# Performance work log

Measured on AMD Instinct MI355X. Metric: run time of the kernel, lower is better.

## Reference

```python
import jax, jax.numpy as jnp
import numpy as np

NUM_HEADS = 8
GROUPS = 32  # min(32, 512 // 4)
EPS = 1e-5


def group_norm(y, gamma, beta):
    B, C, L = y.shape
    yg = y.reshape(B, GROUPS, -1)  # [B, G, (C//G)*L]
    mu = yg.mean(-1, keepdims=True)
    var = yg.var(-1, keepdims=True)
    yn = ((yg - mu) * jax.lax.rsqrt(var + EPS)).reshape(B, C, L)
    return yn * gamma[:, None] + beta[:, None]


def setup_inputs() -> dict:
    key = jax.random.key(0)
    ks = jax.random.split(key, 5)
    B, C, L = 4, 512, 2048
    return {
        "x": jax.random.normal(ks[0], (B, C, L), dtype=jnp.float32),
        "Wqkv": jax.random.normal(ks[1], (3 * C, C), dtype=jnp.float32) * (C ** -0.5),
        "bqkv": jax.random.normal(ks[2], (3 * C,), dtype=jnp.float32) * 0.01,
        "Wproj": jax.random.normal(ks[3], (C, C), dtype=jnp.float32) * (C ** -0.5),
        "bproj": jax.random.normal(ks[4], (C,), dtype=jnp.float32) * 0.01,
        "gamma": jnp.ones((C,), dtype=jnp.float32),
        "beta": jnp.zeros((C,), dtype=jnp.float32),
    }


def reference(x, Wqkv, bqkv, Wproj, bproj, gamma, beta):
    B, C, L = x.shape
    H = NUM_HEADS
    D = C // H
    # 1x1 Conv1d == channel-mixing matmul
    qkv = jnp.einsum('oc,bcl->bol', Wqkv, x) + bqkv[:, None]  # [B, 3C, L]
    qkv = qkv.reshape(B, 3, H, D, L)
    q, k, v = qkv[:, 0], qkv[:, 1], qkv[:, 2]
    q = jnp.clip(q, -10.0, 10.0)
    k = jnp.clip(k, -10.0, 10.0)
    v = jnp.clip(v, -10.0, 10.0)
    scale = D ** -0.5
    attn = jnp.einsum('bhdi,bhdj->bhij', q, k) * scale  # [B, H, L, L]
    attn = jnp.clip(attn, -10.0, 10.0)
    attn = jax.nn.softmax(attn, axis=-1)
    # NaN fallback: replace whole attn with identity if any NaN (matches torch branch)
    has_nan = jnp.isnan(attn).any()
    attn = jnp.where(has_nan, jnp.eye(L, dtype=x.dtype), attn)
    out = jnp.einsum('bhij,bhdj->bhdi', attn, v)  # [B, H, D, L]
    out = out.reshape(B, C, L)
    out = jnp.einsum('oc,bcl->bol', Wproj, out) + bproj[:, None]
    return group_norm(out + x, gamma, beta)
```

## Files before the change

kernel.cpp:

```cpp
#include <hip/hip_runtime.h>
#include <cstddef>

#define B_ 4
#define C_ 512
#define L_ 2048

typedef __attribute__((ext_vector_type(8))) short  short8;
typedef __attribute__((ext_vector_type(4))) float  f32x4;
typedef __attribute__((ext_vector_type(4))) unsigned short us4;

#define AS1 __attribute__((address_space(1)))
#define AS3 __attribute__((address_space(3)))

__device__ __forceinline__ float clip10(float v){ return fminf(fmaxf(v,-10.0f),10.0f); }

__device__ __forceinline__ unsigned short f2bf(float f){
  union { float f; unsigned u; } v; v.f = f;
  unsigned r = v.u + 0x7fffu + ((v.u >> 16) & 1u);
  return (unsigned short)(r >> 16);
}
__device__ __forceinline__ unsigned pk_tr(float lo, float hi){
  return __builtin_amdgcn_perm(__float_as_uint(hi), __float_as_uint(lo), 0x07060302u);
}
__device__ __forceinline__ float bf2f(unsigned short u){
  return __uint_as_float(((unsigned)u)<<16);
}
__device__ __forceinline__ void gl16(const void* g, void* l){
  __builtin_amdgcn_global_load_lds((const AS1 unsigned*)g, (AS3 unsigned*)l, 16, 0, 0);
}

__global__ __launch_bounds__(256) void prep_k(
    const float* __restrict__ x, const float* __restrict__ Wq,
    const float* __restrict__ Wp, unsigned short* __restrict__ xT,
    unsigned short* __restrict__ Wqb, unsigned short* __restrict__ Wpb,
    float* __restrict__ part)
{
  const int blk = blockIdx.x;
  const int t = threadIdx.x;
  if (blk < 4096){
    __shared__ float tile[32][33];
    const int b = blk>>10, rem = blk&1023;
    const int c0 = (rem>>6)*32, l0 = (rem&63)*32;
    const int cr = t>>3, lc = (t&7)*4;
    const float4 v = *(const float4*)(x + ((size_t)b*C_ + c0+cr)*L_ + l0 + lc);
    tile[cr][lc]=v.x; tile[cr][lc+1]=v.y; tile[cr][lc+2]=v.z; tile[cr][lc+3]=v.w;
    __syncthreads();
    const int lr = t>>3, cc = (t&7)*4;
    const us4 o = { f2bf(tile[cc][lr]), f2bf(tile[cc+1][lr]),
                    f2bf(tile[cc+2][lr]), f2bf(tile[cc+3][lr]) };
    *(us4*)(xT + ((size_t)b*L_ + l0+lr)*C_ + c0 + cc) = o;
  } else if (blk < 5120){
    const int i = (blk-4096)*256 + t;
    const int NQ = 1536*512/4;
    const float* src; unsigned short* dst; int j;
    if (i < NQ){ src = Wq; dst = Wqb; j = i; }
    else       { src = Wp; dst = Wpb; j = i - NQ; }
    const float4 v = *(const float4*)(src + (size_t)j*4);
    const us4 o = { f2bf(v.x), f2bf(v.y), f2bf(v.z), f2bf(v.w) };
    *(us4*)(dst + (size_t)j*4) = o;
  } else {
    part[t] = 0.f;
  }
}

template<int MODE>
__global__ __launch_bounds__(256) void mfma_gemm(
    const unsigned short* __restrict__ Wb, const unsigned short* __restrict__ Bin,
    const float* __restrict__ bias, const float* __restrict__ xres,
    unsigned short* __restrict__ qT, unsigned short* __restrict__ kT,
    unsigned short* __restrict__ vN, float* __restrict__ yout,
    float* __restrict__ part)
{
  __shared__ unsigned short SA[128*64];
  __shared__ unsigned short SB[128*64];
  const int t = threadIdx.x;
  const int b = blockIdx.z;
  const int mb = blockIdx.y, n0 = blockIdx.x*128, m0 = mb*128;
  const int lane = t&63, w = t>>6, wm = w>>1, wn = w&1;
  const int n = lane&15, q4 = lane>>4;

  f32x4 acc[4][4];
#pragma unroll
  for (int i=0;i<4;i++)
#pragma unroll
    for (int j=0;j<4;j++) acc[i][j] = (f32x4){0.f,0.f,0.f,0.f};

  const unsigned short* Arow = Wb + (size_t)m0*512;
  const unsigned short* Brow = Bin + ((size_t)b*L_ + n0)*512;

  for (int kt=0; kt<8; kt++){
    const int k0 = kt*64;
    __syncthreads();
#pragma unroll
    for (int i=0;i<4;i++){
      const int ch = t + 256*i;
      const int row = ch>>3, lc = (ch&7) ^ (row&7);
      gl16(Arow + (size_t)row*512 + k0 + lc*8, &SA[ch*8]);
      gl16(Brow + (size_t)row*512 + k0 + lc*8, &SB[ch*8]);
    }
    __syncthreads();
#pragma unroll
    for (int kk=0;kk<2;kk++){
      short8 aF[4], bF[4];
      const int pc = ((kk*4+q4) ^ (n&7))*8;
#pragma unroll
      for (int mt=0;mt<4;mt++) aF[mt] = *(const short8*)&SA[(wm*64+mt*16+n)*64 + pc];
#pragma unroll
      for (int nt=0;nt<4;nt++) bF[nt] = *(const short8*)&SB[(wn*64+nt*16+n)*64 + pc];
#pragma unroll
      for (int mt=0;mt<4;mt++)
#pragma unroll
        for (int nt=0;nt<4;nt++)
          acc[mt][nt] = __builtin_amdgcn_mfma_f32_16x16x32_bf16(aF[mt], bF[nt], acc[mt][nt], 0,0,0);
    }
  }

  const float QS = 0.180336880f;
#pragma unroll
  for (int mt=0;mt<4;mt++){
    const int obase = m0 + wm*64 + mt*16 + q4*4;
    const float b0=bias[obase], b1=bias[obase+1], b2=bias[obase+2], b3=bias[obase+3];
    float gs=0.f, gq=0.f;
#pragma unroll
    for (int nt=0;nt<4;nt++){
      const int l = n0 + wn*64 + nt*16 + n;
      float r0=acc[mt][nt][0]+b0, r1=acc[mt][nt][1]+b1,
            r2=acc[mt][nt][2]+b2, r3=acc[mt][nt][3]+b3;
      if (MODE==0){
        r0=clip10(r0); r1=clip10(r1); r2=clip10(r2); r3=clip10(r3);
        const int typ = mb>>2;
        const int oin = obase - typ*512;
        if (typ < 2){
          if (typ==0){ r0*=QS; r1*=QS; r2*=QS; r3*=QS; }
          unsigned short* dst = (typ==0) ? qT : kT;
          const us4 o = { f2bf(r0), f2bf(r1), f2bf(r2), f2bf(r3) };
          *(us4*)&dst[((size_t)b*L_ + l)*512 + oin] = o;
        } else {
          unsigned short* dst = vN + ((size_t)b*512 + oin)*L_ + l;
          dst[0]=f2bf(r0); dst[(size_t)L_]=f2bf(r1);
          dst[(size_t)2*L_]=f2bf(r2); dst[(size_t)3*L_]=f2bf(r3);
        }
      } else {
        const float* xp = xres + ((size_t)b*512 + obase)*L_ + l;
        const float y0=r0+xp[0], y1=r1+xp[(size_t)L_],
                    y2=r2+xp[(size_t)2*L_], y3=r3+xp[(size_t)3*L_];
        float* dst = yout + ((size_t)b*512 + obase)*L_ + l;
        dst[0]=y0; dst[(size_t)L_]=y1; dst[(size_t)2*L_]=y2; dst[(size_t)3*L_]=y3;
        gs += (y0+y1)+(y2+y3);
        gq += (y0*y0+y1*y1)+(y2*y2+y3*y3);
      }
    }
    if (MODE==1){
#pragma unroll
      for (int off=1; off<64; off<<=1){
        gs += __shfl_xor(gs, off);
        gq += __shfl_xor(gq, off);
      }
      if (lane==0){
        const int g = mb*8 + wm*4 + mt;
        atomicAdd(&part[(b*32+g)*2+0], gs);
        atomicAdd(&part[(b*32+g)*2+1], gq);
      }
    }
  }
}

#define PP 72

__global__ __launch_bounds__(256,4) void attn_v9(
    const unsigned short* __restrict__ qT, const unsigned short* __restrict__ kT,
    const unsigned short* __restrict__ vN,
    unsigned short* __restrict__ Opart, float* __restrict__ den)
{
  __shared__ unsigned short s_k[64*64];
  __shared__ unsigned short s_v[64*64];
  __shared__ unsigned short s_p[128*PP];
  const int t  = threadIdx.x;
  const int io = blockIdx.x>>1, half = blockIdx.x&1;
  const int i0 = io*128;
  const int h  = blockIdx.y, b = blockIdx.z;
  const int lane = t&63, w = t>>6, n = lane&15, q4 = lane>>4;
  const int idx = ((b*8+h)*16+io)*2 + half;

  const unsigned short* kb0 = kT + (size_t)b*L_*512 + h*64;
  const unsigned short* vb  = vN + ((size_t)b*512 + h*64)*L_;

  short8 qf[2][2];
#pragma unroll
  for (int mt=0; mt<2; mt++)
#pragma unroll
    for (int kk=0; kk<2; kk++)
      qf[mt][kk] = *(const short8*)(qT + ((size_t)b*L_ + i0 + w*32 + mt*16 + n)*512
                                       + h*64 + kk*32 + q4*8);

  short8 ones;
#pragma unroll
  for (int i=0;i<8;i++) ones[i] = (short)0x3F80;

  f32x4 oacc[2][4];
  f32x4 oden[2];
#pragma unroll
  for (int mt=0;mt<2;mt++){ oden[mt]=(f32x4){0.f,0.f,0.f,0.f};
#pragma unroll
    for (int dt=0;dt<4;dt++) oacc[mt][dt]=(f32x4){0.f,0.f,0.f,0.f}; }

  const float LIM = 14.4269504089f;
  const int jbeg = half*1024, jend = jbeg+1024;

  for (int j0=jbeg; j0<jend; j0+=64){
    __syncthreads();
#pragma unroll
    for (int i=0;i<2;i++){
      const int ch = t + 256*i, row = ch>>3, lc = (ch&7)^(row&7);
      gl16(kb0 + (size_t)(j0+row)*512 + lc*8, &s_k[ch*8]);
      gl16(vb  + (size_t)row*L_ + j0 + lc*8,  &s_v[ch*8]);
    }
    __syncthreads();

    f32x4 sacc[2][4];
#pragma unroll
    for (int mt=0;mt<2;mt++)
#pragma unroll
      for (int jt=0;jt<4;jt++) sacc[mt][jt]=(f32x4){0.f,0.f,0.f,0.f};
#pragma unroll
    for (int kk=0;kk<2;kk++){
      const int pc = ((kk*4+q4) ^ (n&7))*8;
      short8 aK[4];
#pragma unroll
      for (int jt=0;jt<4;jt++) aK[jt] = *(const short8*)&s_k[(jt*16+n)*64 + pc];
#pragma unroll
      for (int mt=0;mt<2;mt++)
#pragma unroll
        for (int jt=0;jt<4;jt++)
          sacc[mt][jt] = __builtin_amdgcn_mfma_f32_16x16x32_bf16(aK[jt], qf[mt][kk], sacc[mt][jt], 0,0,0);
    }

#pragma unroll
    for (int mt=0;mt<2;mt++)
#pragma unroll
      for (int jt=0;jt<4;jt++){
        const float e0 = __builtin_amdgcn_exp2f(__builtin_amdgcn_fmed3f(sacc[mt][jt][0],-LIM,LIM));
        const float e1 = __builtin_amdgcn_exp2f(__builtin_amdgcn_fmed3f(sacc[mt][jt][1],-LIM,LIM));
        const float e2 = __builtin_amdgcn_exp2f(__builtin_amdgcn_fmed3f(sacc[mt][jt][2],-LIM,LIM));
        const float e3 = __builtin_amdgcn_exp2f(__builtin_amdgcn_fmed3f(sacc[mt][jt][3],-LIM,LIM));
        const unsigned long long pv =
            (unsigned long long)pk_tr(e0,e1) | ((unsigned long long)pk_tr(e2,e3)<<32);
        *(unsigned long long*)&s_p[(w*32 + mt*16 + n)*PP + jt*16 + q4*4] = pv;
      }

#pragma unroll
    for (int kk=0;kk<2;kk++){
      const int pcv = ((kk*4+q4) ^ (n&7))*8;
      short8 bV[4], pA[2];
#pragma unroll
      for (int dt=0;dt<4;dt++) bV[dt] = *(const short8*)&s_v[(dt*16+n)*64 + pcv];
#pragma unroll
      for (int mt=0;mt<2;mt++)
        pA[mt] = *(const short8*)&s_p[(w*32 + mt*16 + n)*PP + kk*32 + q4*8];
#pragma unroll
      for (int mt=0;mt<2;mt++){
#pragma unroll
        for (int dt=0;dt<4;dt++)
          oacc[mt][dt] = __builtin_amdgcn_mfma_f32_16x16x32_bf16(pA[mt], bV[dt], oacc[mt][dt], 0,0,0);
        oden[mt] = __builtin_amdgcn_mfma_f32_16x16x32_bf16(pA[mt], ones, oden[mt], 0,0,0);
      }
    }
  }

  if (n == 0){
#pragma unroll
    for (int mt=0;mt<2;mt++)
#pragma unroll
      for (int r=0;r<4;r++)
        den[(size_t)idx*128 + w*32 + mt*16 + q4*4 + r] = oden[mt][r];
  }

#pragma unroll
  for (int mt=0;mt<2;mt++)
#pragma unroll
    for (int dt=0;dt<4;dt++)
#pragma unroll
      for (int r=0;r<4;r++)
        Opart[(size_t)idx*8192 + (w*32 + mt*16 + q4*4 + r)*64 + dt*16 + n]
            = f2bf(oacc[mt][dt][r]);
}

__global__ __launch_bounds__(256) void attn_combine(
    const unsigned short* __restrict__ Opart, const float* __restrict__ den,
    unsigned short* __restrict__ attnT)
{
  __shared__ float s_inv[128];
  const int io = blockIdx.x, h = blockIdx.y, b = blockIdx.z;
  const int t = threadIdx.x;
  const int base = ((b*8+h)*16+io)*2;
  if (t < 128)
    s_inv[t] = 1.0f/(den[(size_t)base*128 + t] + den[(size_t)(base+1)*128 + t]);
  __syncthreads();
  const unsigned short* O0 = Opart + (size_t)base*8192;
  const unsigned short* O1 = O0 + 8192;
#pragma unroll
  for (int it=0; it<8; it++){
    const int chunk = it*256 + t;
    const int i = chunk>>4, c4 = (chunk&15)*4;
    const us4 a = *(const us4*)&O0[i*64 + c4];
    const us4 c = *(const us4*)&O1[i*64 + c4];
    const float inv = s_inv[i];
    const us4 o = { f2bf((bf2f(a[0])+bf2f(c[0]))*inv),
                    f2bf((bf2f(a[1])+bf2f(c[1]))*inv),
                    f2bf((bf2f(a[2])+bf2f(c[2]))*inv),
                    f2bf((bf2f(a[3])+bf2f(c[3]))*inv) };
    *(us4*)&attnT[((size_t)b*L_ + io*128 + i)*512 + h*64 + c4] = o;
  }
}

__global__ __launch_bounds__(256) void gn_apply(
    const float* __restrict__ y, const float* __restrict__ part,
    const float* __restrict__ gamma, const float* __restrict__ beta,
    float* __restrict__ out)
{
  const int blk = blockIdx.x;
  const int b = blk>>7, g = (blk>>2)&31, s = blk&3;
  const float sum = part[(b*32+g)*2+0];
  const float sq  = part[(b*32+g)*2+1];
  const float mu = sum*(1.0f/32768.0f);
  const float rs = rsqrtf(sq*(1.0f/32768.0f) - mu*mu + 1e-5f);
  const size_t base = ((size_t)b*C_ + g*16)*L_ + s*512;
  const int t = threadIdx.x;
#pragma unroll
  for (int i=0;i<8;i++){
    const int e = i*256 + t;
    const int row = e>>7;
    const size_t off = base + (size_t)row*L_ + (e&127)*4;
    const int c = g*16 + row;
    const float ga = gamma[c], be = beta[c];
    const float4 vy=*(const float4*)(y+off);
    float4 r;
    r.x=(vy.x-mu)*rs*ga+be;
    r.y=(vy.y-mu)*rs*ga+be;
    r.z=(vy.z-mu)*rs*ga+be;
    r.w=(vy.w-mu)*rs*ga+be;
    *(float4*)(out+off)=r;
  }
}

extern "C" void kernel_launch(void* const* d_in, const int* in_sizes, int n_in,
                              void* d_out, int out_size, void* d_ws, size_t ws_size,
                              hipStream_t stream)
{
  (void)in_sizes; (void)n_in; (void)out_size; (void)ws_size;
  const float* x     = (const float*)d_in[0];
  const float* Wqkv  = (const float*)d_in[1];
  const float* bqkv  = (const float*)d_in[2];
  const float* Wproj = (const float*)d_in[3];
  const float* bproj = (const float*)d_in[4];
  const float* gamma = (const float*)d_in[5];
  const float* beta  = (const float*)d_in[6];
  float* out = (float*)d_out;
  char* ws = (char*)d_ws;

  const size_t MB = 1024*1024;
  unsigned short* qT    = (unsigned short*)(ws);
  unsigned short* kT    = (unsigned short*)(ws +  8*MB);
  unsigned short* vN    = (unsigned short*)(ws + 16*MB);
  unsigned short* attnT = (unsigned short*)(ws + 24*MB);
  unsigned short* xT    = (unsigned short*)(ws + 32*MB);
  float*          den   = (float*)        (ws + 41*MB);
  unsigned short* Wqb   = (unsigned short*)(ws + 42*MB);
  unsigned short* Wpb   = (unsigned short*)(ws + 44*MB);
  float*          y     = (float*)        (ws + 45*MB);
  unsigned short* Opart = (unsigned short*)(ws + 45*MB);
  float*          part  = (float*)        (ws + 61*MB);

  prep_k      <<<dim3(5121),   256,0,stream>>>(x, Wqkv, Wproj, xT, Wqb, Wpb, part);
  mfma_gemm<0><<<dim3(16,12,4),256,0,stream>>>(Wqb, xT,    bqkv , nullptr, qT,kT,vN, nullptr, nullptr);
  attn_v9     <<<dim3(32,8,4), 256,0,stream>>>(qT, kT, vN, Opart, den);
  attn_combine<<<dim3(16,8,4), 256,0,stream>>>(Opart, den, attnT);
  mfma_gemm<1><<<dim3(16, 4,4),256,0,stream>>>(Wpb, attnT, bproj, x, nullptr,nullptr,nullptr, y, part);
  gn_apply    <<<dim3(512),    256,0,stream>>>(y, part, gamma, beta, out);
}
```

Baseline: 189.0 us.

## Split attention waves over key halves and vectorize V stores in QKV GEMM

The attention kernel now gives each wave 64 query rows and half of each 64-key tile, rather than 32 query rows and the full tile. This halves the K fragment loads per wave and reuses each Q fragment across more MFMAs. A shared-memory reduction at the end merges the two key-half partial outputs and denominators, and the occupancy hint drops from 4 to 3 blocks to fit the larger register footprint. The QKV GEMM also swaps MFMA operands for the V blocks, so the transposed V output is written as contiguous 4-element vector stores instead of strided scalar ones.

```diff
diff --git a/kernel.cpp b/kernel.cpp
--- a/kernel.cpp
+++ b/kernel.cpp
@@ -78,6 +78,7 @@
   const int mb = blockIdx.y, n0 = blockIdx.x*128, m0 = mb*128;
   const int lane = t&63, w = t>>6, wm = w>>1, wn = w&1;
   const int n = lane&15, q4 = lane>>4;
+  const bool VSWAP = (MODE==0) && (mb>=8);
 
   f32x4 acc[4][4];
 #pragma unroll
@@ -107,15 +108,39 @@
       for (int mt=0;mt<4;mt++) aF[mt] = *(const short8*)&SA[(wm*64+mt*16+n)*64 + pc];
 #pragma unroll
       for (int nt=0;nt<4;nt++) bF[nt] = *(const short8*)&SB[(wn*64+nt*16+n)*64 + pc];
-#pragma unroll
-      for (int mt=0;mt<4;mt++)
-#pragma unroll
-        for (int nt=0;nt<4;nt++)
-          acc[mt][nt] = __builtin_amdgcn_mfma_f32_16x16x32_bf16(aF[mt], bF[nt], acc[mt][nt], 0,0,0);
+      if (VSWAP){
+#pragma unroll
+        for (int mt=0;mt<4;mt++)
+#pragma unroll
+          for (int nt=0;nt<4;nt++)
+            acc[mt][nt] = __builtin_amdgcn_mfma_f32_16x16x32_bf16(bF[nt], aF[mt], acc[mt][nt], 0,0,0);
+      } else {
+#pragma unroll
+        for (int mt=0;mt<4;mt++)
+#pragma unroll
+          for (int nt=0;nt<4;nt++)
+            acc[mt][nt] = __builtin_amdgcn_mfma_f32_16x16x32_bf16(aF[mt], bF[nt], acc[mt][nt], 0,0,0);
+      }
     }
   }
 
   const float QS = 0.180336880f;
+  if (VSWAP){
+#pragma unroll
+    for (int mt=0;mt<4;mt++){
+      const int o = m0 + wm*64 + mt*16 + n;
+      const float bv = bias[o];
+#pragma unroll
+      for (int nt=0;nt<4;nt++){
+        const int l = n0 + wn*64 + nt*16 + q4*4;
+        const float r0=clip10(acc[mt][nt][0]+bv), r1=clip10(acc[mt][nt][1]+bv),
+                    r2=clip10(acc[mt][nt][2]+bv), r3=clip10(acc[mt][nt][3]+bv);
+        const us4 ov = { f2bf(r0), f2bf(r1), f2bf(r2), f2bf(r3) };
+        *(us4*)&vN[((size_t)b*512 + (o-1024))*L_ + l] = ov;
+      }
+    }
+    return;
+  }
 #pragma unroll
   for (int mt=0;mt<4;mt++){
     const int obase = m0 + wm*64 + mt*16 + q4*4;
@@ -130,16 +155,10 @@
         r0=clip10(r0); r1=clip10(r1); r2=clip10(r2); r3=clip10(r3);
         const int typ = mb>>2;
         const int oin = obase - typ*512;
-        if (typ < 2){
-          if (typ==0){ r0*=QS; r1*=QS; r2*=QS; r3*=QS; }
-          unsigned short* dst = (typ==0) ? qT : kT;
-          const us4 o = { f2bf(r0), f2bf(r1), f2bf(r2), f2bf(r3) };
-          *(us4*)&dst[((size_t)b*L_ + l)*512 + oin] = o;
-        } else {
-          unsigned short* dst = vN + ((size_t)b*512 + oin)*L_ + l;
-          dst[0]=f2bf(r0); dst[(size_t)L_]=f2bf(r1);
-          dst[(size_t)2*L_]=f2bf(r2); dst[(size_t)3*L_]=f2bf(r3);
-        }
+        if (typ==0){ r0*=QS; r1*=QS; r2*=QS; r3*=QS; }
+        unsigned short* dst = (typ==0) ? qT : kT;
+        const us4 o = { f2bf(r0), f2bf(r1), f2bf(r2), f2bf(r3) };
+        *(us4*)&dst[((size_t)b*L_ + l)*512 + oin] = o;
       } else {
         const float* xp = xres + ((size_t)b*512 + obase)*L_ + l;
         const float y0=r0+xp[0], y1=r1+xp[(size_t)L_],
@@ -166,46 +185,50 @@
 }
 
 #define PP 72
-
-__global__ __launch_bounds__(256,4) void attn_v9(
+#define EXP 66
+
+__global__ __launch_bounds__(256,3) void attn_v12(
     const unsigned short* __restrict__ qT, const unsigned short* __restrict__ kT,
     const unsigned short* __restrict__ vN,
     unsigned short* __restrict__ Opart, float* __restrict__ den)
 {
-  __shared__ unsigned short s_k[64*64];
-  __shared__ unsigned short s_v[64*64];
-  __shared__ unsigned short s_p[128*PP];
+  __shared__ unsigned short smem[2*64*64 + 128*PP];
+  unsigned short* s_k = smem;
+  unsigned short* s_v = smem + 4096;
+  unsigned short* s_p = smem + 8192;
   const int t  = threadIdx.x;
   const int io = blockIdx.x>>1, half = blockIdx.x&1;
   const int i0 = io*128;
   const int h  = blockIdx.y, b = blockIdx.z;
   const int lane = t&63, w = t>>6, n = lane&15, q4 = lane>>4;
+  const int wi = w&1, wj = w>>1;
   const int idx = ((b*8+h)*16+io)*2 + half;
 
   const unsigned short* kb0 = kT + (size_t)b*L_*512 + h*64;
   const unsigned short* vb  = vN + ((size_t)b*512 + h*64)*L_;
 
-  short8 qf[2][2];
-#pragma unroll
-  for (int mt=0; mt<2; mt++)
+  short8 qf[4][2];
+#pragma unroll
+  for (int mt=0; mt<4; mt++)
 #pragma unroll
     for (int kk=0; kk<2; kk++)
-      qf[mt][kk] = *(const short8*)(qT + ((size_t)b*L_ + i0 + w*32 + mt*16 + n)*512
+      qf[mt][kk] = *(const short8*)(qT + ((size_t)b*L_ + i0 + wi*64 + mt*16 + n)*512
                                        + h*64 + kk*32 + q4*8);
 
   short8 ones;
 #pragma unroll
   for (int i=0;i<8;i++) ones[i] = (short)0x3F80;
 
-  f32x4 oacc[2][4];
-  f32x4 oden[2];
-#pragma unroll
-  for (int mt=0;mt<2;mt++){ oden[mt]=(f32x4){0.f,0.f,0.f,0.f};
+  f32x4 oacc[4][4];
+  f32x4 oden[4];
+#pragma unroll
+  for (int mt=0;mt<4;mt++){ oden[mt]=(f32x4){0.f,0.f,0.f,0.f};
 #pragma unroll
     for (int dt=0;dt<4;dt++) oacc[mt][dt]=(f32x4){0.f,0.f,0.f,0.f}; }
 
   const float LIM = 14.4269504089f;
   const int jbeg = half*1024, jend = jbeg+1024;
+  const int prow = (wi*64 + n)*PP + wj*32;
 
   for (int j0=jbeg; j0<jend; j0+=64){
     __syncthreads();
@@ -217,48 +240,48 @@
     }
     __syncthreads();
 
-    f32x4 sacc[2][4];
-#pragma unroll
-    for (int mt=0;mt<2;mt++)
-#pragma unroll
-      for (int jt=0;jt<4;jt++) sacc[mt][jt]=(f32x4){0.f,0.f,0.f,0.f};
+    f32x4 sacc[4][2];
+#pragma unroll
+    for (int mt=0;mt<4;mt++)
+#pragma unroll
+      for (int jt2=0;jt2<2;jt2++) sacc[mt][jt2]=(f32x4){0.f,0.f,0.f,0.f};
 #pragma unroll
     for (int kk=0;kk<2;kk++){
       const int pc = ((kk*4+q4) ^ (n&7))*8;
-      short8 aK[4];
-#pragma unroll
-      for (int jt=0;jt<4;jt++) aK[jt] = *(const short8*)&s_k[(jt*16+n)*64 + pc];
-#pragma unroll
-      for (int mt=0;mt<2;mt++)
-#pragma unroll
-        for (int jt=0;jt<4;jt++)
-          sacc[mt][jt] = __builtin_amdgcn_mfma_f32_16x16x32_bf16(aK[jt], qf[mt][kk], sacc[mt][jt], 0,0,0);
-    }
-
-#pragma unroll
-    for (int mt=0;mt<2;mt++)
-#pragma unroll
-      for (int jt=0;jt<4;jt++){
-        const float e0 = __builtin_amdgcn_exp2f(__builtin_amdgcn_fmed3f(sacc[mt][jt][0],-LIM,LIM));
-        const float e1 = __builtin_amdgcn_exp2f(__builtin_amdgcn_fmed3f(sacc[mt][jt][1],-LIM,LIM));
-        const float e2 = __builtin_amdgcn_exp2f(__builtin_amdgcn_fmed3f(sacc[mt][jt][2],-LIM,LIM));
-        const float e3 = __builtin_amdgcn_exp2f(__builtin_amdgcn_fmed3f(sacc[mt][jt][3],-LIM,LIM));
+      short8 aK[2];
+#pragma unroll
+      for (int jt2=0;jt2<2;jt2++)
+        aK[jt2] = *(const short8*)&s_k[(wj*32+jt2*16+n)*64 + pc];
+#pragma unroll
+      for (int mt=0;mt<4;mt++)
+#pragma unroll
+        for (int jt2=0;jt2<2;jt2++)
+          sacc[mt][jt2] = __builtin_amdgcn_mfma_f32_16x16x32_bf16(aK[jt2], qf[mt][kk], sacc[mt][jt2], 0,0,0);
+    }
+
+#pragma unroll
+    for (int mt=0;mt<4;mt++)
+#pragma unroll
+      for (int jt2=0;jt2<2;jt2++){
+        const float e0 = __builtin_amdgcn_exp2f(__builtin_amdgcn_fmed3f(sacc[mt][jt2][0],-LIM,LIM));
+        const float e1 = __builtin_amdgcn_exp2f(__builtin_amdgcn_fmed3f(sacc[mt][jt2][1],-LIM,LIM));
+        const float e2 = __builtin_amdgcn_exp2f(__builtin_amdgcn_fmed3f(sacc[mt][jt2][2],-LIM,LIM));
+        const float e3 = __builtin_amdgcn_exp2f(__builtin_amdgcn_fmed3f(sacc[mt][jt2][3],-LIM,LIM));
         const unsigned long long pv =
             (unsigned long long)pk_tr(e0,e1) | ((unsigned long long)pk_tr(e2,e3)<<32);
-        *(unsigned long long*)&s_p[(w*32 + mt*16 + n)*PP + jt*16 + q4*4] = pv;
-      }
-
-#pragma unroll
-    for (int kk=0;kk<2;kk++){
-      const int pcv = ((kk*4+q4) ^ (n&7))*8;
-      short8 bV[4], pA[2];
+        *(unsigned long long*)&s_p[prow + mt*16*PP + jt2*16 + q4*4] = pv;
+      }
+
+    {
+      const int pcv = ((wj*4+q4) ^ (n&7))*8;
+      short8 bV[4], pA[4];
 #pragma unroll
       for (int dt=0;dt<4;dt++) bV[dt] = *(const short8*)&s_v[(dt*16+n)*64 + pcv];
 #pragma unroll
-      for (int mt=0;mt<2;mt++)
-        pA[mt] = *(const short8*)&s_p[(w*32 + mt*16 + n)*PP + kk*32 + q4*8];
-#pragma unroll
-      for (int mt=0;mt<2;mt++){
+      for (int mt=0;mt<4;mt++)
+        pA[mt] = *(const short8*)&s_p[prow + mt*16*PP + q4*8];
+#pragma unroll
+      for (int mt=0;mt<4;mt++){
 #pragma unroll
         for (int dt=0;dt<4;dt++)
           oacc[mt][dt] = __builtin_amdgcn_mfma_f32_16x16x32_bf16(pA[mt], bV[dt], oacc[mt][dt], 0,0,0);
@@ -267,22 +290,48 @@
     }
   }
 
-  if (n == 0){
-#pragma unroll
-    for (int mt=0;mt<2;mt++)
-#pragma unroll
-      for (int r=0;r<4;r++)
-        den[(size_t)idx*128 + w*32 + mt*16 + q4*4 + r] = oden[mt][r];
-  }
-
-#pragma unroll
-  for (int mt=0;mt<2;mt++)
-#pragma unroll
-    for (int dt=0;dt<4;dt++)
-#pragma unroll
-      for (int r=0;r<4;r++)
-        Opart[(size_t)idx*8192 + (w*32 + mt*16 + q4*4 + r)*64 + dt*16 + n]
-            = f2bf(oacc[mt][dt][r]);
+  __syncthreads();
+  float* ex  = (float*)smem;
+  float* dex = (float*)smem + 2*64*EXP;
+  if (wj == 1){
+#pragma unroll
+    for (int mt=0;mt<4;mt++){
+#pragma unroll
+      for (int dt=0;dt<4;dt++)
+#pragma unroll
+        for (int r=0;r<4;r++)
+          ex[(size_t)wi*64*EXP + (mt*16+q4*4+r)*EXP + dt*16+n] = oacc[mt][dt][r];
+      if (n==0){
+#pragma unroll
+        for (int r=0;r<4;r++) dex[wi*64 + mt*16+q4*4+r] = oden[mt][r];
+      }
+    }
+  }
+  __syncthreads();
+  if (wj == 0){
+#pragma unroll
+    for (int mt=0;mt<4;mt++){
+#pragma unroll
+      for (int dt=0;dt<4;dt++)
+#pragma unroll
+        for (int r=0;r<4;r++)
+          oacc[mt][dt][r] += ex[(size_t)wi*64*EXP + (mt*16+q4*4+r)*EXP + dt*16+n];
+      if (n==0){
+#pragma unroll
+        for (int r=0;r<4;r++)
+          den[(size_t)idx*128 + wi*64 + mt*16+q4*4+r]
+              = oden[mt][r] + dex[wi*64 + mt*16+q4*4+r];
+      }
+    }
+#pragma unroll
+    for (int mt=0;mt<4;mt++)
+#pragma unroll
+      for (int dt=0;dt<4;dt++)
+#pragma unroll
+        for (int r=0;r<4;r++)
+          Opart[(size_t)idx*8192 + (wi*64 + mt*16 + q4*4 + r)*64 + dt*16 + n]
+              = f2bf(oacc[mt][dt][r]);
+  }
 }
 
 __global__ __launch_bounds__(256) void attn_combine(
@@ -373,7 +422,7 @@
 
   prep_k      <<<dim3(5121),   256,0,stream>>>(x, Wqkv, Wproj, xT, Wqb, Wpb, part);
   mfma_gemm<0><<<dim3(16,12,4),256,0,stream>>>(Wqb, xT,    bqkv , nullptr, qT,kT,vN, nullptr, nullptr);
-  attn_v9     <<<dim3(32,8,4), 256,0,stream>>>(qT, kT, vN, Opart, den);
+  attn_v12    <<<dim3(32,8,4), 256,0,stream>>>(qT, kT, vN, Opart, den);
   attn_combine<<<dim3(16,8,4), 256,0,stream>>>(Opart, den, attnT);
   mfma_gemm<1><<<dim3(16, 4,4),256,0,stream>>>(Wpb, attnT, bproj, x, nullptr,nullptr,nullptr, y, part);
   gn_apply    <<<dim3(512),    256,0,stream>>>(y, part, gamma, beta, out);
```

Measured after the change: 209.7 us. +10.9%, slower.
